# Kernel optimization log

Measured on AMD Instinct MI355X. Metric: run time of the kernel, lower is better.

Reference implementation:

```python
import jax, jax.numpy as jnp
import numpy as np

N, IN_CHN, MDIM, ATT_D, NUM_CLS = 100000, 1024, 512, 128, 2
NUM_GROUP, INST_PER_GROUP = 8, 4
GROUP_SIZE = N // NUM_GROUP


def setup_inputs() -> dict:
    key = jax.random.key(0)
    ks = jax.random.split(key, 8)
    def w(k, shape, fan):
        return (jax.random.normal(k, shape, jnp.float32) / np.sqrt(fan)).astype(jnp.float32)
    return {
        "index_chunk_list": jax.random.randint(ks[0], (NUM_GROUP, GROUP_SIZE), 0, N),
        "tfeat_tensor": jax.random.normal(ks[1], (N, IN_CHN), jnp.float32),
        # DimReduction: Linear(1024 -> mDim) + ReLU (numLayer_Res = 0)
        "W1": w(ks[2], (MDIM, IN_CHN), IN_CHN), "b1": jnp.zeros((MDIM,), jnp.float32),
        # Attention: Linear(mDim -> 128), tanh, Linear(128 -> 1)
        "Wa1": w(ks[3], (ATT_D, MDIM), MDIM), "ba1": jnp.zeros((ATT_D,), jnp.float32),
        "Wa2": w(ks[4], (1, ATT_D), ATT_D), "ba2": jnp.zeros((1,), jnp.float32),
        # Classifier_1fc: Linear(mDim -> num_cls)  (dropout=0 -> identity)
        "Wc": w(ks[5], (NUM_CLS, MDIM), MDIM), "bc": jnp.zeros((NUM_CLS,), jnp.float32),
    }


def _group_forward(idx, tfeat, W1, b1, Wa1, ba1, Wa2, ba2, Wc, bc):
    # idx: [S] instance indices for one pseudo-bag
    sub = jnp.take(tfeat, idx, axis=0)                       # [S, in_chn]  gather
    mid = jax.nn.relu(sub @ W1.T + b1)                       # [S, m]       DimReduction
    a = jnp.tanh(mid @ Wa1.T + ba1) @ Wa2.T + ba2            # [S, 1]       Attention logits
    a = jax.nn.softmax(a[:, 0], axis=0)                      # [S]          softmax over instances
    att = mid * a[:, None]                                   # [S, m]       einsum('ns,n->ns')
    bag = att.sum(axis=0)                                    # [m]          attention-weighted sum
    pred = bag @ Wc.T + bc                                    # [C]          bag-level logits
    # get_cam_1d: per-instance logits from classifier weight only (no bias)
    cam = jax.nn.softmax(att @ Wc.T, axis=1)                  # [S, C]
    order = jnp.argsort(-cam[:, -1])                          # descending sort on last-class prob
    topk = jnp.concatenate([order[:INST_PER_GROUP], order[-INST_PER_GROUP:]])
    maxmin = jnp.take(mid, topk, axis=0)                      # [2k, m]  MaxMinS distill feats
    return pred, maxmin


def reference(index_chunk_list, tfeat_tensor, W1, b1, Wa1, ba1, Wa2, ba2, Wc, bc):
    f = jax.vmap(_group_forward, in_axes=(0,) + (None,) * 9)
    slide_sub_preds, slide_pseudo_feat = f(index_chunk_list, tfeat_tensor,
                                           W1, b1, Wa1, ba1, Wa2, ba2, Wc, bc)
    # [numGroup, num_cls], [numGroup, 2*instance_per_group, mDim]
    return slide_sub_preds, slide_pseudo_feat
```

## Files before the change

### kernel.cpp

```cpp
#include <hip/hip_runtime.h>
#include <stdint.h>

#define N_TOT 100000
#define IN_CHN 1024
#define MDIM 512
#define ATT_D 128
#define NUM_GROUP 8
#define GROUP_SIZE 12500
#define SEGR 98

typedef __bf16 bf16x8 __attribute__((ext_vector_type(8)));
typedef float f32x4 __attribute__((ext_vector_type(4)));
typedef unsigned short u16x8 __attribute__((ext_vector_type(8)));

__device__ __forceinline__ unsigned short f2bf(float x){
  union { float f; unsigned u; } v; v.f = x;
  unsigned r = v.u + 0x7fffu + ((v.u >> 16) & 1u);
  return (unsigned short)(r >> 16);
}
__device__ __forceinline__ float bf2f(unsigned short h){
  union { unsigned u; float f; } v; v.u = ((unsigned)h) << 16; return v.f;
}
__device__ __forceinline__ void gload16(const void* g, void* l){
  __builtin_amdgcn_global_load_lds(
      (const __attribute__((address_space(1))) unsigned int*)g,
      (__attribute__((address_space(3))) unsigned int*)l, 16, 0, 0);
}

__global__ __launch_bounds__(256) void kconv(const float* __restrict__ W1,
                                             const float* __restrict__ Wa1,
                                             unsigned short* __restrict__ W1b,
                                             unsigned short* __restrict__ Wa1b){
  int i = blockIdx.x * 256 + threadIdx.x;
  if (i < MDIM * IN_CHN) W1b[i] = f2bf(W1[i]);
  else {
    int j = i - MDIM * IN_CHN;
    if (j < ATT_D * MDIM) Wa1b[j] = f2bf(Wa1[j]);
  }
}

__global__ __launch_bounds__(256) void kgemm_mid(const int* __restrict__ idxf,
                                                 const float* __restrict__ tfeat,
                                                 const unsigned short* __restrict__ W1b,
                                                 const float* __restrict__ b1,
                                                 unsigned short* __restrict__ midb){
  __shared__ alignas(16) float Af0[128 * 32];
  __shared__ alignas(16) float Af1[128 * 32];
  __shared__ alignas(16) unsigned short Bsm[128 * 64];
  __shared__ int gsm[128];
  int tid = threadIdx.x;
  int bidg = blockIdx.x;
  int tile = (bidg & 7) * 391 + (bidg >> 3);
  int bn = tile & 3, bm = tile >> 2;
  int m0 = bm * 128, n0 = bn * 128;
  if (tid < 128){ int r = m0 + tid; gsm[tid] = idxf[r < N_TOT ? r : 0]; }
  __syncthreads();

  int w = tid >> 6, l = tid & 63;
  int l16 = tid & 15, hi = (tid >> 4) & 3;
  int wm = tid >> 7, wn = (tid >> 6) & 1;

  const float* asrc[4];
  const unsigned short* bsrc[4];
  int adsto[4], bdsto[4];
  int scw = (l & 7) ^ (l >> 3);
  #pragma unroll
  for (int q = 0; q < 4; q++){
    int rowl = q * 32 + w * 8 + (l >> 3);
    asrc[q] = tfeat + (size_t)gsm[rowl] * IN_CHN + scw * 4;
    bsrc[q] = W1b + (size_t)(n0 + rowl) * IN_CHN + scw * 8;
    adsto[q] = (q * 32 + w * 8) * 32;
    bdsto[q] = (q * 32 + w * 8) * 64;
  }

  f32x4 acc[4][4];
  #pragma unroll
  for (int a = 0; a < 4; a++)
    #pragma unroll
    for (int b = 0; b < 4; b++) acc[a][b] = (f32x4){0.f, 0.f, 0.f, 0.f};

  int r7 = l16 & 7;

  for (int s = 0; s < 16; s++){
    __syncthreads();
    #pragma unroll
    for (int q = 0; q < 4; q++){
      gload16(asrc[q] + s * 64,      &Af0[adsto[q]]);
      gload16(asrc[q] + s * 64 + 32, &Af1[adsto[q]]);
      gload16(bsrc[q] + s * 64,      &Bsm[bdsto[q]]);
    }
    __syncthreads();

    #pragma unroll
    for (int ks = 0; ks < 2; ks++){
      const float* At = ks ? Af1 : Af0;
      bf16x8 af[4], bfr[4];
      #pragma unroll
      for (int a = 0; a < 4; a++){
        int row = wm * 64 + a * 16 + l16;
        f32x4 lo  = *(const f32x4*)&At[row * 32 + (((2 * hi) ^ r7) << 2)];
        f32x4 hi4 = *(const f32x4*)&At[row * 32 + (((2 * hi + 1) ^ r7) << 2)];
        bf16x8 pk;
        pk[0] = (__bf16)lo[0]; pk[1] = (__bf16)lo[1]; pk[2] = (__bf16)lo[2]; pk[3] = (__bf16)lo[3];
        pk[4] = (__bf16)hi4[0]; pk[5] = (__bf16)hi4[1]; pk[6] = (__bf16)hi4[2]; pk[7] = (__bf16)hi4[3];
        af[a] = pk;
      }
      #pragma unroll
      for (int b = 0; b < 4; b++){
        int row = wn * 64 + b * 16 + l16;
        bfr[b] = *(const bf16x8*)&Bsm[row * 64 + (((ks * 4 + hi) ^ r7) << 3)];
      }
      #pragma unroll
      for (int a = 0; a < 4; a++)
        #pragma unroll
        for (int b = 0; b < 4; b++)
          acc[a][b] = __builtin_amdgcn_mfma_f32_16x16x32_bf16(af[a], bfr[b], acc[a][b], 0, 0, 0);
    }
  }

  #pragma unroll
  for (int b = 0; b < 4; b++){
    int col = n0 + wn * 64 + b * 16 + l16;
    float bias = b1[col];
    #pragma unroll
    for (int a = 0; a < 4; a++){
      int rbase = m0 + wm * 64 + a * 16 + hi * 4;
      #pragma unroll
      for (int q = 0; q < 4; q++){
        int row = rbase + q;
        if (row < N_TOT){
          float v = acc[a][b][q] + bias;
          midb[(size_t)row * MDIM + col] = f2bf(fmaxf(v, 0.f));
        }
      }
    }
  }
}

__global__ __launch_bounds__(256) void kattn(const unsigned short* __restrict__ midb,
                                             const unsigned short* __restrict__ Wa1b,
                                             const float* __restrict__ ba1,
                                             const float* __restrict__ Wa2,
                                             const float* __restrict__ ba2,
                                             const float* __restrict__ Wc,
                                             float* __restrict__ lv,
                                             float* __restrict__ tv){
  __shared__ alignas(16) unsigned short Asm[128 * 64];
  __shared__ alignas(16) unsigned short Bsm[128 * 64];
  __shared__ float dsh[512];
  __shared__ float part[128][2];
  int tid = threadIdx.x;
  int m0 = blockIdx.x * 128;
  for (int i = tid; i < 512; i += 256) dsh[i] = Wc[512 + i] - Wc[i];

  int w = tid >> 6, l = tid & 63;
  int l16 = tid & 15, hi = (tid >> 4) & 3;
  int wm = tid >> 7, wn = (tid >> 6) & 1;
  int scw = (l & 7) ^ (l >> 3);

  const unsigned short *asrc[4], *bsrc[4];
  int dsto[4];
  #pragma unroll
  for (int q = 0; q < 4; q++){
    int rowl = q * 32 + w * 8 + (l >> 3);
    asrc[q] = midb + (size_t)(m0 + rowl) * MDIM + scw * 8;
    bsrc[q] = Wa1b + (size_t)rowl * MDIM + scw * 8;
    dsto[q] = (q * 32 + w * 8) * 64;
  }

  f32x4 acc[4][4];
  #pragma unroll
  for (int a = 0; a < 4; a++)
    #pragma unroll
    for (int b = 0; b < 4; b++) acc[a][b] = (f32x4){0.f, 0.f, 0.f, 0.f};
  int r7 = l16 & 7;

  int rt = tid >> 1, kh = tid & 1;
  int rt7 = rt & 7;
  float t = 0.f;

  for (int s = 0; s < 8; s++){
    __syncthreads();
    #pragma unroll
    for (int q = 0; q < 4; q++){
      gload16(asrc[q] + s * 64, &Asm[dsto[q]]);
      gload16(bsrc[q] + s * 64, &Bsm[dsto[q]]);
    }
    __syncthreads();
    #pragma unroll
    for (int ks = 0; ks < 2; ks++){
      bf16x8 af[4], bfr[4];
      #pragma unroll
      for (int a = 0; a < 4; a++){
        int row = wm * 64 + a * 16 + l16;
        af[a] = *(const bf16x8*)&Asm[row * 64 + (((ks * 4 + hi) ^ r7) << 3)];
      }
      #pragma unroll
      for (int b = 0; b < 4; b++){
        int row = wn * 64 + b * 16 + l16;
        bfr[b] = *(const bf16x8*)&Bsm[row * 64 + (((ks * 4 + hi) ^ r7) << 3)];
      }
      #pragma unroll
      for (int a = 0; a < 4; a++)
        #pragma unroll
        for (int b = 0; b < 4; b++)
          acc[a][b] = __builtin_amdgcn_mfma_f32_16x16x32_bf16(af[a], bfr[b], acc[a][b], 0, 0, 0);
    }
    #pragma unroll
    for (int j = 0; j < 4; j++){
      int gc = kh * 4 + j;
      u16x8 v = *(const u16x8*)&Asm[rt * 64 + ((gc ^ rt7) << 3)];
      int kb = s * 64 + gc * 8;
      #pragma unroll
      for (int e = 0; e < 8; e++) t += bf2f((unsigned short)v[e]) * dsh[kb + e];
    }
  }
  t += __shfl_xor(t, 1);
  if (kh == 0){
    int row = m0 + rt;
    if (row < N_TOT) tv[row] = t;
  }
  #pragma unroll
  for (int a = 0; a < 4; a++){
    #pragma unroll
    for (int q = 0; q < 4; q++){
      float v = 0.f;
      #pragma unroll
      for (int b = 0; b < 4; b++){
        int col = wn * 64 + b * 16 + l16;
        v += tanhf(acc[a][b][q] + ba1[col]) * Wa2[col];
      }
      #pragma unroll
      for (int off = 1; off < 16; off <<= 1) v += __shfl_xor(v, off);
      if (l16 == 0) part[wm * 64 + a * 16 + hi * 4 + q][wn] = v;
    }
  }
  __syncthreads();
  if (tid < 128){
    int row = m0 + tid;
    if (row < N_TOT) lv[row] = part[tid][0] + part[tid][1] + ba2[0];
  }
}

__global__ __launch_bounds__(256) void kselect(const float* __restrict__ lv,
                                               const float* __restrict__ tv,
                                               float* __restrict__ maxlw, float* __restrict__ Zw,
                                               int* __restrict__ cand,
                                               float* __restrict__ w){
  __shared__ float keys[GROUP_SIZE];
  __shared__ float candk[4096];
  __shared__ int   candi[4096];
  __shared__ float rk[256];
  __shared__ int ri[256];
  __shared__ int rs[256];
  __shared__ float sbc;
  int g = blockIdx.x, tid = threadIdx.x;
  const float* lg = lv + (size_t)g * GROUP_SIZE;
  const float* tg = tv + (size_t)g * GROUP_SIZE;

  float mx = -1e30f;
  for (int i = tid; i < GROUP_SIZE; i += 256) mx = fmaxf(mx, lg[i]);
  rk[tid] = mx; __syncthreads();
  for (int s = 128; s > 0; s >>= 1){ if (tid < s) rk[tid] = fmaxf(rk[tid], rk[tid + s]); __syncthreads(); }
  if (tid == 0) sbc = rk[0];
  __syncthreads();
  float maxl = sbc;

  float z = 0.f;
  for (int i = tid; i < GROUP_SIZE; i += 256){
    float ez = expf(lg[i] - maxl);
    z += ez;
    keys[i] = ez * tg[i];
  }
  rk[tid] = z; __syncthreads();
  for (int s = 128; s > 0; s >>= 1){ if (tid < s) rk[tid] += rk[tid + s]; __syncthreads(); }
  if (tid == 0){ maxlw[g] = maxl; Zw[g] = rk[0]; }
  __syncthreads();
  float invZ = 1.0f / rk[0];
  for (int i = tid; i < GROUP_SIZE; i += 256)
    w[(size_t)g * GROUP_SIZE + i] = expf(lg[i] - maxl) * invZ;
  __syncthreads();

  {
    float tk[16]; int tix[16];
    #pragma unroll
    for (int j = 0; j < 16; j++){ tk[j] = -1e30f; tix[j] = 0x7fffffff; }
    for (int i = tid; i < GROUP_SIZE; i += 256){
      float ck = keys[i];
      if (ck > tk[15]){
        int ci = i;
        #pragma unroll
        for (int j = 0; j < 16; j++){
          bool ins = ck > tk[j];
          float nk = ins ? ck : tk[j]; int ni = ins ? ci : tix[j];
          float ok = ins ? tk[j] : ck; int oi = ins ? tix[j] : ci;
          tk[j] = nk; tix[j] = ni; ck = ok; ci = oi;
        }
      }
    }
    #pragma unroll
    for (int j = 0; j < 16; j++){ candk[tid * 16 + j] = tk[j]; candi[tid * 16 + j] = tix[j]; }
  }
  __syncthreads();
  for (int it = 0; it < 16; it++){
    float bk = -1e30f; int bi = 0x7fffffff; int bs = -1;
    for (int jj = tid; jj < 4096; jj += 256){
      float k = candk[jj]; int ix = candi[jj];
      if (k > bk || (k == bk && ix < bi)){ bk = k; bi = ix; bs = jj; }
    }
    rk[tid] = bk; ri[tid] = bi; rs[tid] = bs; __syncthreads();
    for (int s = 128; s > 0; s >>= 1){
      if (tid < s){
        if (rk[tid + s] > rk[tid] || (rk[tid + s] == rk[tid] && ri[tid + s] < ri[tid])){
          rk[tid] = rk[tid + s]; ri[tid] = ri[tid + s]; rs[tid] = rs[tid + s];
        }
      }
      __syncthreads();
    }
    if (tid == 0){ cand[g * 32 + it] = ri[0]; candk[rs[0]] = -1e30f; }
    __syncthreads();
  }

  {
    float tk[16]; int tix[16];
    #pragma unroll
    for (int j = 0; j < 16; j++){ tk[j] = 1e30f; tix[j] = -1; }
    for (int i = tid; i < GROUP_SIZE; i += 256){
      float ck = keys[i];
      if (ck <= tk[15]){
        int ci = i;
        #pragma unroll
        for (int j = 0; j < 16; j++){
          bool ins = ck <= tk[j];
          float nk = ins ? ck : tk[j]; int ni = ins ? ci : tix[j];
          float ok = ins ? tk[j] : ck; int oi = ins ? tix[j] : ci;
          tk[j] = nk; tix[j] = ni; ck = ok; ci = oi;
        }
      }
    }
    #pragma unroll
    for (int j = 0; j < 16; j++){ candk[tid * 16 + j] = tk[j]; candi[tid * 16 + j] = tix[j]; }
  }
  __syncthreads();
  for (int it = 0; it < 16; it++){
    float bk = 1e30f; int bi = -1; int bs = -1;
    for (int jj = tid; jj < 4096; jj += 256){
      float k = candk[jj]; int ix = candi[jj];
      if (k < bk || (k == bk && ix > bi)){ bk = k; bi = ix; bs = jj; }
    }
    rk[tid] = bk; ri[tid] = bi; rs[tid] = bs; __syncthreads();
    for (int s = 128; s > 0; s >>= 1){
      if (tid < s){
        if (rk[tid + s] < rk[tid] || (rk[tid + s] == rk[tid] && ri[tid + s] > ri[tid])){
          rk[tid] = rk[tid + s]; ri[tid] = ri[tid + s]; rs[tid] = rs[tid + s];
        }
      }
      __syncthreads();
    }
    if (tid == 0){ cand[g * 32 + 16 + it] = ri[0]; candk[rs[0]] = 1e30f; }
    __syncthreads();
  }
}

__global__ __launch_bounds__(256) void kexact(const int* __restrict__ idxf,
                                              const float* __restrict__ tfeat,
                                              const float* __restrict__ W1,
                                              const float* __restrict__ b1,
                                              const float* __restrict__ Wa1,
                                              const float* __restrict__ ba1,
                                              const float* __restrict__ Wa2,
                                              const float* __restrict__ ba2,
                                              const float* __restrict__ Wc,
                                              const int* __restrict__ cand,
                                              const float* __restrict__ maxlw,
                                              float* __restrict__ emid, float* __restrict__ ekey){
  __shared__ float subs[1024];
  __shared__ float midc[512];
  __shared__ float hs[128];
  __shared__ float red[256];
  __shared__ float tsh;
  int bid = blockIdx.x; int g = bid >> 5, c = bid & 31; int tid = threadIdx.x;
  int s = cand[g * 32 + c];
  int inst = idxf[g * GROUP_SIZE + s];
  ((float4*)subs)[tid] = ((const float4*)(tfeat + (size_t)inst * IN_CHN))[tid];
  __syncthreads();

  float a0 = b1[tid], a1 = b1[tid + 256];
  const float4* w0 = (const float4*)(W1 + (size_t)tid * IN_CHN);
  const float4* w1 = (const float4*)(W1 + ((size_t)tid + 256) * IN_CHN);
  const float4* s4 = (const float4*)subs;
  #pragma unroll 4
  for (int k = 0; k < 256; k++){
    float4 sv = s4[k], wva = w0[k], wvb = w1[k];
    a0 += sv.x * wva.x + sv.y * wva.y + sv.z * wva.z + sv.w * wva.w;
    a1 += sv.x * wvb.x + sv.y * wvb.y + sv.z * wvb.z + sv.w * wvb.w;
  }
  a0 = fmaxf(a0, 0.f); a1 = fmaxf(a1, 0.f);
  midc[tid] = a0; midc[tid + 256] = a1;
  size_t eo = (size_t)(g * 32 + c) * MDIM;
  emid[eo + tid] = a0; emid[eo + tid + 256] = a1;
  __syncthreads();

  if (tid < 128){
    const float4* wr = (const float4*)(Wa1 + (size_t)tid * MDIM);
    const float4* m4 = (const float4*)midc;
    float h = ba1[tid];
    #pragma unroll 4
    for (int j = 0; j < 128; j++){
      float4 mv = m4[j], wv = wr[j];
      h += mv.x * wv.x + mv.y * wv.y + mv.z * wv.z + mv.w * wv.w;
    }
    hs[tid] = tanhf(h) * Wa2[tid];
  }
  __syncthreads();

  float tp = midc[tid] * (Wc[512 + tid] - Wc[tid]) + midc[tid + 256] * (Wc[768 + tid] - Wc[256 + tid]);
  red[tid] = tp; __syncthreads();
  for (int st = 128; st > 0; st >>= 1){ if (tid < st) red[tid] += red[tid + st]; __syncthreads(); }
  if (tid == 0) tsh = red[0];
  __syncthreads();
  red[tid] = (tid < 128) ? hs[tid] : 0.f; __syncthreads();
  for (int st = 128; st > 0; st >>= 1){ if (tid < st) red[tid] += red[tid + st]; __syncthreads(); }
  if (tid == 0){
    float lval = red[0] + ba2[0];
    ekey[g * 32 + c] = expf(lval - maxlw[g]) * tsh;
  }
}

__global__ __launch_bounds__(256) void kbag(const unsigned short* __restrict__ midb,
                                            const float* __restrict__ w,
                                            float* __restrict__ bagp){
  __shared__ float wl[SEGR];
  int g = blockIdx.x >> 7, seg = blockIdx.x & 127, tid = threadIdx.x;
  int i0 = seg * SEGR;
  int nr = GROUP_SIZE - i0; if (nr > SEGR) nr = SEGR;
  size_t base = (size_t)g * GROUP_SIZE;
  if (tid < nr) wl[tid] = w[base + i0 + tid];
  __syncthreads();
  float a0 = 0.f, a1 = 0.f;
  const unsigned short* mp = midb + (base + i0) * MDIM + 2 * tid;
  int i = 0;
  for (; i + 2 <= nr; i += 2){
    unsigned pk0 = *(const unsigned*)(mp + (size_t)i * MDIM);
    unsigned pk1 = *(const unsigned*)(mp + (size_t)(i + 1) * MDIM);
    float w0 = wl[i], w1 = wl[i + 1];
    a0 += w0 * bf2f((unsigned short)(pk0 & 0xffff)) + w1 * bf2f((unsigned short)(pk1 & 0xffff));
    a1 += w0 * bf2f((unsigned short)(pk0 >> 16)) + w1 * bf2f((unsigned short)(pk1 >> 16));
  }
  if (i < nr){
    unsigned pk0 = *(const unsigned*)(mp + (size_t)i * MDIM);
    float w0 = wl[i];
    a0 += w0 * bf2f((unsigned short)(pk0 & 0xffff));
    a1 += w0 * bf2f((unsigned short)(pk0 >> 16));
  }
  float* dst = bagp + (size_t)blockIdx.x * MDIM + 2 * tid;
  dst[0] = a0; dst[1] = a1;
}

__global__ __launch_bounds__(256) void kfinal(const float* __restrict__ bagp,
                                              const float* __restrict__ Wc,
                                              const float* __restrict__ bc,
                                              const float* __restrict__ emid,
                                              const float* __restrict__ ekey,
                                              const int* __restrict__ cand,
                                              float* __restrict__ out){
  __shared__ float k32[32];
  __shared__ int s32[32];
  __shared__ int ordv[32];
  __shared__ float r0[256], r1[256];
  int g = blockIdx.x, tid = threadIdx.x;
  if (tid < 32){ k32[tid] = ekey[g * 32 + tid]; s32[tid] = cand[g * 32 + tid]; }
  __syncthreads();
  if (tid == 0){
    unsigned used = 0;
    for (int a = 0; a < 32; a++){
      int best = -1;
      for (int b = 0; b < 32; b++){
        if ((used >> b) & 1u) continue;
        if (best < 0 || k32[b] > k32[best] || (k32[b] == k32[best] && s32[b] < s32[best])) best = b;
      }
      used |= 1u << best;
      ordv[a] = best;
    }
  }
  float p0 = 0.f, p1 = 0.f;
  for (int j = tid; j < 512; j += 256){
    float bv = 0.f;
    for (int s2 = 0; s2 < 128; s2++) bv += bagp[(size_t)(g * 128 + s2) * MDIM + j];
    p0 += bv * Wc[j];
    p1 += bv * Wc[512 + j];
  }
  r0[tid] = p0; r1[tid] = p1; __syncthreads();
  for (int s = 128; s > 0; s >>= 1){ if (tid < s){ r0[tid] += r0[tid + s]; r1[tid] += r1[tid + s]; } __syncthreads(); }
  if (tid == 0){
    out[g * 2 + 0] = r0[0] + bc[0];
    out[g * 2 + 1] = r1[0] + bc[1];
  }
  __syncthreads();
  for (int p = 0; p < 8; p++){
    int cc = ordv[p < 4 ? p : 24 + p];
    const float* src = emid + (size_t)(g * 32 + cc) * MDIM;
    float* dst = out + 16 + (size_t)(g * 8 + p) * MDIM;
    for (int j = tid; j < 512; j += 256) dst[j] = src[j];
  }
}

extern "C" void kernel_launch(void* const* d_in, const int* in_sizes, int n_in,
                              void* d_out, int out_size, void* d_ws, size_t ws_size,
                              hipStream_t stream){
  const int*   idxf = (const int*)d_in[0];
  const float* tfeat= (const float*)d_in[1];
  const float* W1   = (const float*)d_in[2];
  const float* b1   = (const float*)d_in[3];
  const float* Wa1  = (const float*)d_in[4];
  const float* ba1  = (const float*)d_in[5];
  const float* Wa2  = (const float*)d_in[6];
  const float* ba2  = (const float*)d_in[7];
  const float* Wc   = (const float*)d_in[8];
  const float* bc   = (const float*)d_in[9];
  float* out = (float*)d_out;
  (void)in_sizes; (void)n_in; (void)out_size; (void)ws_size;

  char* ws = (char*)d_ws;
  size_t off = 0;
  auto alloc = [&](size_t bytes){ void* p = ws + off; off += (bytes + 255) & ~(size_t)255; return p; };
  float* lv    = (float*)alloc((size_t)N_TOT * 4);
  float* tv    = (float*)alloc((size_t)N_TOT * 4);
  float* maxlw = (float*)alloc(NUM_GROUP * 4);
  float* Zw    = (float*)alloc(NUM_GROUP * 4);
  int*   cand  = (int*)alloc(NUM_GROUP * 32 * 4);
  float* ekey  = (float*)alloc(NUM_GROUP * 32 * 4);
  float* emid  = (float*)alloc((size_t)NUM_GROUP * 32 * MDIM * 4);
  float* bagp  = (float*)alloc((size_t)NUM_GROUP * 128 * MDIM * 4);
  unsigned short* W1b  = (unsigned short*)alloc((size_t)MDIM * IN_CHN * 2);
  unsigned short* Wa1b = (unsigned short*)alloc((size_t)ATT_D * MDIM * 2);
  unsigned short* midb = (unsigned short*)alloc((size_t)N_TOT * MDIM * 2);
  float* w = tv;

  kconv<<<2304, 256, 0, stream>>>(W1, Wa1, W1b, Wa1b);
  kgemm_mid<<<3128, 256, 0, stream>>>(idxf, tfeat, W1b, b1, midb);
  kattn<<<782, 256, 0, stream>>>(midb, Wa1b, ba1, Wa2, ba2, Wc, lv, tv);
  kselect<<<8, 256, 0, stream>>>(lv, tv, maxlw, Zw, cand, w);
  kexact<<<256, 256, 0, stream>>>(idxf, tfeat, W1, b1, Wa1, ba1, Wa2, ba2, Wc, cand, maxlw, emid, ekey);
  kbag<<<1024, 256, 0, stream>>>(midb, w, bagp);
  kfinal<<<8, 256, 0, stream>>>(bagp, Wc, bc, emid, ekey, cand, out);
}
```

Measured before the change: 656.8 us.

## Double-buffer LDS tiles in gather GEMM to overlap loads with MFMA

```diff
diff --git a/kernel.cpp b/kernel.cpp
--- a/kernel.cpp
+++ b/kernel.cpp
@@ -44,13 +44,13 @@
                                                  const unsigned short* __restrict__ W1b,
                                                  const float* __restrict__ b1,
                                                  unsigned short* __restrict__ midb){
-  __shared__ alignas(16) float Af0[128 * 32];
-  __shared__ alignas(16) float Af1[128 * 32];
-  __shared__ alignas(16) unsigned short Bsm[128 * 64];
+  __shared__ alignas(16) float A0[128 * 32];
+  __shared__ alignas(16) float A1[128 * 32];
+  __shared__ alignas(16) unsigned short B0[128 * 32];
+  __shared__ alignas(16) unsigned short B1[128 * 32];
   __shared__ int gsm[128];
   int tid = threadIdx.x;
-  int bidg = blockIdx.x;
-  int tile = (bidg & 7) * 391 + (bidg >> 3);
+  int tile = (blockIdx.x & 7) * 391 + (blockIdx.x >> 3);
   int bn = tile & 3, bm = tile >> 2;
   int m0 = bm * 128, n0 = bn * 128;
   if (tid < 128){ int r = m0 + tid; gsm[tid] = idxf[r < N_TOT ? r : 0]; }
@@ -60,17 +60,19 @@
   int l16 = tid & 15, hi = (tid >> 4) & 3;
   int wm = tid >> 7, wn = (tid >> 6) & 1;
 
-  const float* asrc[4];
-  const unsigned short* bsrc[4];
-  int adsto[4], bdsto[4];
-  int scw = (l & 7) ^ (l >> 3);
+  const float* asrc[4]; int adst[4];
   #pragma unroll
   for (int q = 0; q < 4; q++){
     int rowl = q * 32 + w * 8 + (l >> 3);
-    asrc[q] = tfeat + (size_t)gsm[rowl] * IN_CHN + scw * 4;
-    bsrc[q] = W1b + (size_t)(n0 + rowl) * IN_CHN + scw * 8;
-    adsto[q] = (q * 32 + w * 8) * 32;
-    bdsto[q] = (q * 32 + w * 8) * 64;
+    asrc[q] = tfeat + (size_t)gsm[rowl] * IN_CHN + (((l & 7) ^ (l >> 3)) << 2);
+    adst[q] = (q * 32 + w * 8) * 32;
+  }
+  const unsigned short* bsrc[2]; int bdst[2];
+  #pragma unroll
+  for (int q = 0; q < 2; q++){
+    int rowl = q * 64 + w * 16 + (l >> 2);
+    bsrc[q] = W1b + (size_t)(n0 + rowl) * IN_CHN + (((l & 3) ^ ((l >> 3) & 3)) << 3);
+    bdst[q] = (q * 64 + w * 16) * 32;
   }
 
   f32x4 acc[4][4];
@@ -80,42 +82,47 @@
     for (int b = 0; b < 4; b++) acc[a][b] = (f32x4){0.f, 0.f, 0.f, 0.f};
 
   int r7 = l16 & 7;
-
-  for (int s = 0; s < 16; s++){
+  int b3 = (l16 >> 1) & 3;
+
+  auto stage = [&](float* Ax, unsigned short* Bx, int s){
+    #pragma unroll
+    for (int q = 0; q < 4; q++) gload16(asrc[q] + s * 32, Ax + adst[q]);
+    #pragma unroll
+    for (int q = 0; q < 2; q++) gload16(bsrc[q] + s * 32, Bx + bdst[q]);
+  };
+  auto compute = [&](const float* Ax, const unsigned short* Bx){
+    bf16x8 af[4], bfr[4];
+    #pragma unroll
+    for (int a = 0; a < 4; a++){
+      int row = wm * 64 + a * 16 + l16;
+      f32x4 lo  = *(const f32x4*)&Ax[row * 32 + (((2 * hi) ^ r7) << 2)];
+      f32x4 hi4 = *(const f32x4*)&Ax[row * 32 + (((2 * hi + 1) ^ r7) << 2)];
+      bf16x8 pk;
+      pk[0] = (__bf16)lo[0]; pk[1] = (__bf16)lo[1]; pk[2] = (__bf16)lo[2]; pk[3] = (__bf16)lo[3];
+      pk[4] = (__bf16)hi4[0]; pk[5] = (__bf16)hi4[1]; pk[6] = (__bf16)hi4[2]; pk[7] = (__bf16)hi4[3];
+      af[a] = pk;
+    }
+    #pragma unroll
+    for (int b = 0; b < 4; b++){
+      int row = wn * 64 + b * 16 + l16;
+      bfr[b] = *(const bf16x8*)&Bx[row * 32 + ((hi ^ b3) << 3)];
+    }
+    #pragma unroll
+    for (int a = 0; a < 4; a++)
+      #pragma unroll
+      for (int b = 0; b < 4; b++)
+        acc[a][b] = __builtin_amdgcn_mfma_f32_16x16x32_bf16(af[a], bfr[b], acc[a][b], 0, 0, 0);
+  };
+
+  stage(A0, B0, 0);
+  __syncthreads();
+  for (int s2 = 0; s2 < 32; s2 += 2){
+    stage(A1, B1, s2 + 1);
+    compute(A0, B0);
     __syncthreads();
-    #pragma unroll
-    for (int q = 0; q < 4; q++){
-      gload16(asrc[q] + s * 64,      &Af0[adsto[q]]);
-      gload16(asrc[q] + s * 64 + 32, &Af1[adsto[q]]);
-      gload16(bsrc[q] + s * 64,      &Bsm[bdsto[q]]);
-    }
+    if (s2 + 2 < 32) stage(A0, B0, s2 + 2);
+    compute(A1, B1);
     __syncthreads();
-
-    #pragma unroll
-    for (int ks = 0; ks < 2; ks++){
-      const float* At = ks ? Af1 : Af0;
-      bf16x8 af[4], bfr[4];
-      #pragma unroll
-      for (int a = 0; a < 4; a++){
-        int row = wm * 64 + a * 16 + l16;
-        f32x4 lo  = *(const f32x4*)&At[row * 32 + (((2 * hi) ^ r7) << 2)];
-        f32x4 hi4 = *(const f32x4*)&At[row * 32 + (((2 * hi + 1) ^ r7) << 2)];
-        bf16x8 pk;
-        pk[0] = (__bf16)lo[0]; pk[1] = (__bf16)lo[1]; pk[2] = (__bf16)lo[2]; pk[3] = (__bf16)lo[3];
-        pk[4] = (__bf16)hi4[0]; pk[5] = (__bf16)hi4[1]; pk[6] = (__bf16)hi4[2]; pk[7] = (__bf16)hi4[3];
-        af[a] = pk;
-      }
-      #pragma unroll
-      for (int b = 0; b < 4; b++){
-        int row = wn * 64 + b * 16 + l16;
-        bfr[b] = *(const bf16x8*)&Bsm[row * 64 + (((ks * 4 + hi) ^ r7) << 3)];
-      }
-      #pragma unroll
-      for (int a = 0; a < 4; a++)
-        #pragma unroll
-        for (int b = 0; b < 4; b++)
-          acc[a][b] = __builtin_amdgcn_mfma_f32_16x16x32_bf16(af[a], bfr[b], acc[a][b], 0, 0, 0);
-    }
   }
 
   #pragma unroll
```

Result: no change. 669.9 us (+2.0%).
